# Optimization experiments

Hardware: AMD Instinct MI355X
Metric: run time of the kernel (lower is better)

## Reference

```python
import jax, jax.numpy as jnp
import numpy as np

N = 20000       # nodes per graph
E = 320000      # edges per graph (avg degree 16)
R = 8           # num_relations
B = 2           # batch of graphs
DIMS = [128, 256, 256, 128]  # in -> hidden -> hidden -> out
SLOPE = 0.2     # LeakyReLU negative slope


def setup_inputs() -> dict:
    key = jax.random.key(0)
    ks = jax.random.split(key, 12)
    inp = {
        "x": jax.random.normal(ks[0], (B, N, DIMS[0]), dtype=jnp.float32),
        "edge_index": jax.random.randint(ks[1], (B, 2, E), 0, N, dtype=jnp.int32),
        "edge_type": jax.random.randint(ks[2], (B, E), 0, R, dtype=jnp.int32),
    }
    for l in range(3):
        cin, cout = DIMS[l], DIMS[l + 1]
        s = 1.0 / np.sqrt(cin)
        inp[f"W{l}"] = jax.random.normal(ks[3 + 3 * l], (R, cin, cout), jnp.float32) * s
        inp[f"root{l}"] = jax.random.normal(ks[4 + 3 * l], (cin, cout), jnp.float32) * s
        inp[f"b{l}"] = jnp.zeros((cout,), jnp.float32)
    return inp


def _rgcn_layer(h, src, dst, etype, W, root, b):
    """One RGCNConv (per-relation mean aggregation) on a single graph.
    h: (N,Cin), src/dst/etype: (E,), W: (R,Cin,Cout), root: (Cin,Cout), b: (Cout,)
    """
    # transform every node by every relation weight once: (N,R,Cout)
    h_rel = jnp.einsum('nc,rcd->nrd', h, W)
    # per-edge message: gather source node transformed by that edge's relation
    msg = h_rel[src, etype]                               # (E,Cout)
    # per-(target-node, relation) mean, as in PyG's per-relation propagate
    seg = dst * R + etype                                 # (E,)
    sums = jax.ops.segment_sum(msg, seg, num_segments=N * R)
    cnt = jax.ops.segment_sum(jnp.ones((msg.shape[0],), h.dtype), seg,
                              num_segments=N * R)
    mean = sums / jnp.maximum(cnt, 1.0)[:, None]          # (N*R,Cout)
    agg = mean.reshape(N, R, -1).sum(axis=1)              # (N,Cout)
    return agg + h @ root + b


def reference(x, edge_index, edge_type, W0, root0, b0, W1, root1, b1, W2, root2, b2):
    params = [(W0, root0, b0), (W1, root1, b1), (W2, root2, b2)]

    def single(xg, ei, et):
        src, dst = ei[0], ei[1]
        h = xg
        for (W, root, b) in params:
            h = _rgcn_layer(h, src, dst, et, W, root, b)
            h = jnp.where(h > 0, h, SLOPE * h)  # LeakyReLU(0.2); dropout=identity (eval)
        return h

    return jax.vmap(single)(x, edge_index, edge_type)
```

## Files before the change

kernel.cpp:

```cpp
#include <hip/hip_runtime.h>
#include <hip/hip_bf16.h>

#define NN 20000
#define EE 320000
#define RR 8
#define NR (NN * RR)
#define NB 40
#define SCAP 640

typedef float f32x4 __attribute__((ext_vector_type(4)));
typedef short s16x8 __attribute__((ext_vector_type(8)));

__device__ __forceinline__ unsigned short f2bf(float f) {
  unsigned u = __builtin_bit_cast(unsigned, f);
  unsigned r = u + 0x7FFFu + ((u >> 16) & 1u);
  return (unsigned short)(r >> 16);
}
__device__ __forceinline__ float bf2f(unsigned short u) {
  return __builtin_bit_cast(float, (unsigned)u << 16);
}
__device__ __forceinline__ void gload_lds16(const void* g, void* l) {
  __builtin_amdgcn_global_load_lds(
      (const __attribute__((address_space(1))) unsigned*)g,
      (__attribute__((address_space(3))) unsigned*)l, 16, 0, 0);
}

__global__ void k_count(const int* __restrict__ ei, const int* __restrict__ et,
                        int* __restrict__ cnt) {
  int e = blockIdx.x * blockDim.x + threadIdx.x;
  int g = e >= EE;
  int el = e - g * EE;
  int d = ei[(size_t)g * 2 * EE + EE + el];
  int t = et[(size_t)g * EE + el];
  atomicAdd(&cnt[(size_t)g * NR + d * RR + t], 1);
}

__global__ __launch_bounds__(1024) void k_scan1(const int* __restrict__ cnt,
                                                int* __restrict__ off,
                                                int* __restrict__ btot) {
  int g = blockIdx.y, b = blockIdx.x;
  const int* c = cnt + (size_t)g * NR;
  int* o = off + (size_t)g * NR;
  __shared__ int wsum[16];
  int lane = threadIdx.x & 63, w = threadIdx.x >> 6;
  int i = b * 4096 + (int)threadIdx.x * 4;
  int4 v = {0, 0, 0, 0};
  if (i + 3 < NR) v = *(const int4*)&c[i];
  else {
    if (i < NR) v.x = c[i];
    if (i + 1 < NR) v.y = c[i + 1];
    if (i + 2 < NR) v.z = c[i + 2];
  }
  int s0 = v.x, s1 = s0 + v.y, s2 = s1 + v.z, s3 = s2 + v.w;
  int s = s3;
  for (int d = 1; d < 64; d <<= 1) {
    int t = __shfl_up(s, d);
    if (lane >= d) s += t;
  }
  if (lane == 63) wsum[w] = s;
  __syncthreads();
  if (threadIdx.x < 16) {
    int ws = wsum[threadIdx.x];
    for (int d = 1; d < 16; d <<= 1) {
      int t = __shfl_up(ws, d);
      if ((int)threadIdx.x >= d) ws += t;
    }
    wsum[threadIdx.x] = ws;
  }
  __syncthreads();
  int excl = (w > 0 ? wsum[w - 1] : 0) + (s - s3);
  if (i < NR) o[i] = excl;
  if (i + 1 < NR) o[i + 1] = excl + s0;
  if (i + 2 < NR) o[i + 2] = excl + s1;
  if (i + 3 < NR) o[i + 3] = excl + s2;
  if (threadIdx.x == 0) btot[g * NB + b] = wsum[15];
}

__global__ void k_scan2(const int* __restrict__ btot, int* __restrict__ bof) {
  int g = threadIdx.x >> 6, lane = threadIdx.x & 63;
  int v = (lane < NB) ? btot[g * NB + lane] : 0;
  int s = v;
  for (int d = 1; d < 64; d <<= 1) {
    int t = __shfl_up(s, d);
    if (lane >= d) s += t;
  }
  if (lane < NB) bof[g * NB + lane] = s - v;
}

__global__ __launch_bounds__(1024) void k_scan3(int* __restrict__ off,
                                                const int* __restrict__ bof) {
  int g = blockIdx.y;
  int add = bof[g * NB + blockIdx.x];
  int i = blockIdx.x * 4096 + (int)threadIdx.x * 4;
  int* o = off + (size_t)g * NR;
  if (i + 3 < NR) {
    int4 v = *(const int4*)&o[i];
    v.x += add; v.y += add; v.z += add; v.w += add;
    *(int4*)&o[i] = v;
  } else {
    for (int j = i; j < NR; ++j) o[j] += add;
  }
}

__global__ void k_scatter(const int* __restrict__ ei, const int* __restrict__ et,
                          int* __restrict__ off, int* __restrict__ ssrc) {
  int e = blockIdx.x * blockDim.x + threadIdx.x;
  int g = e >= EE;
  int el = e - g * EE;
  int s = ei[(size_t)g * 2 * EE + el];
  int d = ei[(size_t)g * 2 * EE + EE + el];
  int t = et[(size_t)g * EE + el];
  int pos = atomicAdd(&off[(size_t)g * NR + d * RR + t], 1);
  ssrc[(size_t)g * EE + pos] = s;
}

__global__ void k_cvt(const float* __restrict__ x, unsigned short* __restrict__ hX) {
  int i = (blockIdx.x * blockDim.x + threadIdx.x) * 4;
  if (i >= 2 * NN * 128) return;
  int g = i >= NN * 128;
  int il = i - g * NN * 128;
  float4 v = *(const float4*)&x[i];
  ushort4 o;
  o.x = f2bf(v.x); o.y = f2bf(v.y); o.z = f2bf(v.z); o.w = f2bf(v.w);
  *(ushort4*)&hX[(size_t)g * NN * 256 + il] = o;
}

__global__ void k_btf(const float* __restrict__ W, const float* __restrict__ root,
                      unsigned short* __restrict__ btf, int Cin, int Cout,
                      int Ktot) {
  int idx = blockIdx.x * blockDim.x + threadIdx.x;
  if (idx >= Cout * Ktot) return;
  int j = idx & 7;
  int lane = (idx >> 3) & 63;
  int kk = (idx >> 9) & 1;
  int t = idx >> 10;
  int fr = t % (Cout / 16);
  int s = t / (Cout / 16);
  int co = fr * 16 + (lane & 15);
  int k = s * 64 + kk * 32 + (lane >> 4) * 8 + j;
  int r = k / Cin, ci = k - r * Cin;
  float v = (r < RR) ? W[((size_t)r * Cin + ci) * Cout + co]
                     : root[(size_t)ci * Cout + co];
  btf[idx] = f2bf(v);
}

#define LOADB(bb, s)                                                           \
  _Pragma("unroll") for (int kk = 0; kk < 2; ++kk)                             \
      _Pragma("unroll") for (int f = 0; f < 4; ++f) bb[kk][f] =                \
          *(const s16x8*)(btl +                                                \
                          (size_t)(((s) * (COUT / 16) + wn16 + f) * 2 + kk) *  \
                              512);

#define COPYB()                                                                \
  _Pragma("unroll") for (int kk = 0; kk < 2; ++kk)                             \
      _Pragma("unroll") for (int f = 0; f < 4; ++f) bc[kk][f] = bn[kk][f];

#define MFMA_STEP_C(Ab, c, bb)                                                 \
  do {                                                                         \
    _Pragma("unroll") for (int kk = 0; kk < 2; ++kk) {                         \
      s16x8 a[MF];                                                             \
      _Pragma("unroll") for (int f = 0; f < MF; ++f) {                         \
        int row = wm + f * 16 + (lane & 15);                                   \
        int colb = kk * 64 + (lane >> 4) * 16;                                 \
        a[f] = *(const s16x8*)((Ab) + (c)*ASTR + row * 128 +                   \
                               (colb ^ ((row & 7) << 4)));                     \
      }                                                                        \
      _Pragma("unroll") for (int fm = 0; fm < MF; ++fm)                        \
          _Pragma("unroll") for (int fn = 0; fn < 4; ++fn)                     \
              acc[fm][fn] = __builtin_amdgcn_mfma_f32_16x16x32_bf16(           \
                  a[fm], bb[kk][fn], acc[fm][fn], 0, 0, 0);                    \
    }                                                                          \
  } while (0)

#define ACC4(u)                                                                \
  {                                                                            \
    faH[c][0] += __builtin_bit_cast(float, (u).x & 0xFFFF0000u);               \
    faL[c][0] += __builtin_bit_cast(float, (u).x << 16);                       \
    faH[c][1] += __builtin_bit_cast(float, (u).y & 0xFFFF0000u);               \
    faL[c][1] += __builtin_bit_cast(float, (u).y << 16);                       \
    faH[c][2] += __builtin_bit_cast(float, (u).z & 0xFFFF0000u);               \
    faL[c][2] += __builtin_bit_cast(float, (u).z << 16);                       \
    faH[c][3] += __builtin_bit_cast(float, (u).w & 0xFFFF0000u);               \
    faL[c][3] += __builtin_bit_cast(float, (u).w << 16);                       \
  }

template <int CIN, int COUT, bool OUTF32>
__global__ __launch_bounds__(256) void k_fused(
    const int* __restrict__ ssrc, const int* __restrict__ off,
    const unsigned short* __restrict__ h, const unsigned short* __restrict__ btf,
    const float* __restrict__ bias, void* __restrict__ outp) {
  constexpr int KTOT = (RR + 1) * CIN;
  constexpr int NS = KTOT / 64;
  constexpr int CH = CIN / 64;
  constexpr int CPT = CIN / 8;
  constexpr int NCH = CPT / 8;
  constexpr int NWN = COUT / 64;
  constexpr int MW = 4 / NWN;
  constexpr int WR = 32 / MW;
  constexpr int MF = WR / 16;
  constexpr int ASTR = 4112;
  __shared__ char As[2][CH * ASTR];
  __shared__ int offs[32][9];
  __shared__ int sseg[SCAP];
  const int tid = threadIdx.x, lane = tid & 63, wave = tid >> 6;
  const int wn = (wave % NWN) * 64;
  const int wn16 = wn >> 4;
  const int wm = (wave / NWN) * WR;
  const int m0 = blockIdx.x * 32;
  const int g = blockIdx.z;
  ssrc += (size_t)g * EE;
  off += (size_t)g * NR;
  h += (size_t)g * NN * 256;

  for (int idx = tid; idx < 32 * 9; idx += 256) {
    int row = idx / 9, j = idx - row * 9;
    int seg0 = (m0 + row) * RR;
    offs[row][j] = (j == 0) ? (seg0 == 0 ? 0 : off[seg0 - 1]) : off[seg0 + j - 1];
  }
  const int segA = m0 * RR;
  const int ebase = (segA == 0) ? 0 : off[segA - 1];
  const int eend = off[(m0 + 32) * RR - 1];
  const int cntE = eend - ebase;
  const bool inl = cntE <= SCAP;
  if (inl)
    for (int i = tid; i < cntE; i += 256) sseg[i] = ssrc[ebase + i];
  __syncthreads();

  f32x4 acc[MF][4] = {};
  const int arow = tid >> 3;
  const int q = tid & 7;
  const int swzA = (arow & 7) << 4;
  const unsigned short* hq = h + q * CPT;
  const unsigned short* btl = btf + lane * 8;

  auto produce = [&](int r, int buf) {
    float faL[NCH][4], faH[NCH][4];
#pragma unroll
    for (int c = 0; c < NCH; ++c)
#pragma unroll
      for (int w = 0; w < 4; ++w) { faL[c][w] = 0.f; faH[c][w] = 0.f; }
    int o0 = offs[arow][r], o1 = offs[arow][r + 1];
    int e = o0;
    for (; e + 1 < o1; e += 2) {
      int sa = inl ? sseg[e - ebase] : ssrc[e];
      int sb = inl ? sseg[e + 1 - ebase] : ssrc[e + 1];
      const unsigned short* pa = hq + (size_t)sa * CIN;
      const unsigned short* pb = hq + (size_t)sb * CIN;
#pragma unroll
      for (int c = 0; c < NCH; ++c) {
        uint4 ua = *(const uint4*)(pa + c * 8);
        uint4 ub = *(const uint4*)(pb + c * 8);
        ACC4(ua);
        ACC4(ub);
      }
    }
    if (e < o1) {
      int sa = inl ? sseg[e - ebase] : ssrc[e];
      const unsigned short* pa = hq + (size_t)sa * CIN;
#pragma unroll
      for (int c = 0; c < NCH; ++c) {
        uint4 ua = *(const uint4*)(pa + c * 8);
        ACC4(ua);
      }
    }
    float inv = 1.0f / fmaxf((float)(o1 - o0), 1.0f);
#pragma unroll
    for (int c = 0; c < NCH; ++c) {
      s16x8 mbv;
#pragma unroll
      for (int w = 0; w < 4; ++w) {
        mbv[2 * w] = (short)f2bf(faL[c][w] * inv);
        mbv[2 * w + 1] = (short)f2bf(faH[c][w] * inv);
      }
      int colb = (q * CPT + c * 8) * 2;
      int ct = colb >> 7;
      int wb = colb & 127;
      *(s16x8*)(As[buf] + ct * ASTR + arow * 128 + (wb ^ swzA)) = mbv;
    }
  };

  auto root_stage = [&]() {
#pragma unroll
    for (int i = 0; i < CH; ++i) {
      int o = i * ASTR + wave * 1024;
      int ob = wave * 1024 + lane * 16;
      int row = (ob >> 7) & 31;
      int wb = ob & 127;
      gload_lds16((const char*)h + ((size_t)(m0 + row) * CIN + i * 64) * 2 +
                      (wb ^ ((row & 7) << 4)),
                  As[RR & 1] + o);
    }
  };

  s16x8 bc[2][4], bn[2][4];
  LOADB(bc, 0);
  produce(0, 0);
  __syncthreads();

  for (int r = 0; r <= RR; ++r) {
    const char* Ab = As[r & 1];
#pragma unroll
    for (int c = 0; c < CH; ++c) {
      int s = r * CH + c;
      if (s + 1 < NS) { LOADB(bn, s + 1); }
      MFMA_STEP_C(Ab, c, bc);
      if (s + 1 < NS) { COPYB(); }
    }
    if (r + 1 < RR) produce(r + 1, (r + 1) & 1);
    else if (r + 1 == RR) root_stage();
    __syncthreads();
  }

#pragma unroll
  for (int fm = 0; fm < MF; ++fm) {
    int rbase = m0 + wm + fm * 16 + (lane >> 4) * 4;
#pragma unroll
    for (int fn = 0; fn < 4; ++fn) {
      int col = wn + fn * 16 + (lane & 15);
      float bv = bias[col];
#pragma unroll
      for (int v = 0; v < 4; ++v) {
        int row = rbase + v;
        float xv = acc[fm][fn][v] + bv;
        xv = xv > 0.f ? xv : 0.2f * xv;
        if constexpr (OUTF32)
          ((float*)outp)[(size_t)g * NN * COUT + (size_t)row * COUT + col] = xv;
        else
          ((unsigned short*)outp)[(size_t)g * NN * 256 + (size_t)row * COUT +
                                  col] = f2bf(xv);
      }
    }
  }
}

extern "C" void kernel_launch(void* const* d_in, const int* in_sizes, int n_in,
                              void* d_out, int out_size, void* d_ws, size_t ws_size,
                              hipStream_t stream) {
  const float* x  = (const float*)d_in[0];
  const int* ei   = (const int*)d_in[1];
  const int* etp  = (const int*)d_in[2];
  const float* W0 = (const float*)d_in[3];
  const float* r0 = (const float*)d_in[4];
  const float* b0 = (const float*)d_in[5];
  const float* W1 = (const float*)d_in[6];
  const float* r1 = (const float*)d_in[7];
  const float* b1 = (const float*)d_in[8];
  const float* W2 = (const float*)d_in[9];
  const float* r2 = (const float*)d_in[10];
  const float* b2 = (const float*)d_in[11];

  char* p = (char*)d_ws;
  unsigned short* hX  = (unsigned short*)p; p += (size_t)2 * NN * 256 * 2;
  unsigned short* h_a = (unsigned short*)p; p += (size_t)2 * NN * 256 * 2;
  int* cnt  = (int*)p; p += (size_t)2 * NR * 4;
  int* off  = (int*)p; p += (size_t)2 * NR * 4;
  int* btot = (int*)p; p += (size_t)2 * NB * 4;
  int* bof  = (int*)p; p += (size_t)2 * NB * 4;
  int* ssrc = (int*)p; p += (size_t)2 * EE * 4;
  unsigned short* bt0 = (unsigned short*)p; p += (size_t)256 * 1152 * 2;
  unsigned short* bt1 = (unsigned short*)p; p += (size_t)256 * 2304 * 2;
  unsigned short* bt2 = (unsigned short*)p; p += (size_t)128 * 2304 * 2;

  k_btf<<<(256 * 1152 + 255) / 256, 256, 0, stream>>>(W0, r0, bt0, 128, 256, 1152);
  k_btf<<<(256 * 2304 + 255) / 256, 256, 0, stream>>>(W1, r1, bt1, 256, 256, 2304);
  k_btf<<<(128 * 2304 + 255) / 256, 256, 0, stream>>>(W2, r2, bt2, 256, 128, 2304);

  (void)hipMemsetAsync(cnt, 0, (size_t)2 * NR * 4, stream);
  k_count<<<2 * EE / 256, 256, 0, stream>>>(ei, etp, cnt);
  k_scan1<<<dim3(NB, 2), 1024, 0, stream>>>(cnt, off, btot);
  k_scan2<<<1, 128, 0, stream>>>(btot, bof);
  k_scan3<<<dim3(NB, 2), 1024, 0, stream>>>(off, bof);
  k_cvt<<<2 * NN * 128 / 4 / 256, 256, 0, stream>>>(x, hX);
  k_scatter<<<2 * EE / 256, 256, 0, stream>>>(ei, etp, off, ssrc);

  k_fused<128, 256, false><<<dim3(625, 1, 2), 256, 0, stream>>>(
      ssrc, off, hX, bt0, b0, h_a);
  k_fused<256, 256, false><<<dim3(625, 1, 2), 256, 0, stream>>>(
      ssrc, off, h_a, bt1, b1, hX);
  k_fused<256, 128, true><<<dim3(625, 1, 2), 256, 0, stream>>>(
      ssrc, off, hX, bt2, b2, d_out);
}
```

Baseline: 387.4 us.

## Process both graphs per block with 512 threads to share weight-fragment loads

Each fused block now covers the same 32-row node tile of both graphs (64 rows, 8 waves), so every B-fragment load of the packed weights serves twice as many MFMA rows. Source indices are pre-shifted into byte offsets in shared memory, and the B double-buffer is ping-ponged across two k-steps instead of being copied each step. In exchange, shared memory and register use per block roughly double and there are half as many blocks, which can lower occupancy and latency hiding for the gather phase.

After: 473.4 us. 22.2% more time.

```diff
diff --git a/kernel.cpp b/kernel.cpp
--- a/kernel.cpp
+++ b/kernel.cpp
@@ -151,10 +151,6 @@
                           (size_t)(((s) * (COUT / 16) + wn16 + f) * 2 + kk) *  \
                               512);
 
-#define COPYB()                                                                \
-  _Pragma("unroll") for (int kk = 0; kk < 2; ++kk)                             \
-      _Pragma("unroll") for (int f = 0; f < 4; ++f) bc[kk][f] = bn[kk][f];
-
 #define MFMA_STEP_C(Ab, c, bb)                                                 \
   do {                                                                         \
     _Pragma("unroll") for (int kk = 0; kk < 2; ++kk) {                         \
@@ -185,7 +181,7 @@
   }
 
 template <int CIN, int COUT, bool OUTF32>
-__global__ __launch_bounds__(256) void k_fused(
+__global__ __launch_bounds__(512) void k_fused(
     const int* __restrict__ ssrc, const int* __restrict__ off,
     const unsigned short* __restrict__ h, const unsigned short* __restrict__ btf,
     const float* __restrict__ bias, void* __restrict__ outp) {
@@ -195,42 +191,48 @@
   constexpr int CPT = CIN / 8;
   constexpr int NCH = CPT / 8;
   constexpr int NWN = COUT / 64;
-  constexpr int MW = 4 / NWN;
-  constexpr int WR = 32 / MW;
+  constexpr int MW = 8 / NWN;
+  constexpr int WR = 64 / MW;
   constexpr int MF = WR / 16;
-  constexpr int ASTR = 4112;
+  constexpr int ASTR = 64 * 128 + 16;
+  constexpr int SH = (CIN == 256) ? 9 : 8;
   __shared__ char As[2][CH * ASTR];
-  __shared__ int offs[32][9];
-  __shared__ int sseg[SCAP];
+  __shared__ int offs[64][9];
+  __shared__ int sseg[2 * SCAP];
   const int tid = threadIdx.x, lane = tid & 63, wave = tid >> 6;
   const int wn = (wave % NWN) * 64;
   const int wn16 = wn >> 4;
   const int wm = (wave / NWN) * WR;
   const int m0 = blockIdx.x * 32;
-  const int g = blockIdx.z;
-  ssrc += (size_t)g * EE;
-  off += (size_t)g * NR;
-  h += (size_t)g * NN * 256;
-
-  for (int idx = tid; idx < 32 * 9; idx += 256) {
+
+  for (int idx = tid; idx < 64 * 9; idx += 512) {
     int row = idx / 9, j = idx - row * 9;
-    int seg0 = (m0 + row) * RR;
-    offs[row][j] = (j == 0) ? (seg0 == 0 ? 0 : off[seg0 - 1]) : off[seg0 + j - 1];
-  }
-  const int segA = m0 * RR;
-  const int ebase = (segA == 0) ? 0 : off[segA - 1];
-  const int eend = off[(m0 + 32) * RR - 1];
-  const int cntE = eend - ebase;
-  const bool inl = cntE <= SCAP;
-  if (inl)
-    for (int i = tid; i < cntE; i += 256) sseg[i] = ssrc[ebase + i];
+    const int* offg = off + (size_t)(row >> 5) * NR;
+    int seg0 = (m0 + (row & 31)) * RR;
+    offs[row][j] = (j == 0) ? (seg0 == 0 ? 0 : offg[seg0 - 1]) : offg[seg0 + j - 1];
+  }
+  const int eb0 = (m0 == 0) ? 0 : off[m0 * RR - 1];
+  const int ee0 = off[(m0 + 32) * RR - 1];
+  const int eb1 = (m0 == 0) ? 0 : off[NR + m0 * RR - 1];
+  const int ee1 = off[NR + (m0 + 32) * RR - 1];
+  const bool inl0 = (ee0 - eb0) <= SCAP, inl1 = (ee1 - eb1) <= SCAP;
+  if (inl0)
+    for (int i = tid; i < ee0 - eb0; i += 512) sseg[i] = ssrc[eb0 + i] << SH;
+  if (inl1)
+    for (int i = tid; i < ee1 - eb1; i += 512)
+      sseg[SCAP + i] = ssrc[(size_t)EE + eb1 + i] << SH;
   __syncthreads();
 
   f32x4 acc[MF][4] = {};
   const int arow = tid >> 3;
   const int q = tid & 7;
   const int swzA = (arow & 7) << 4;
-  const unsigned short* hq = h + q * CPT;
+  const int gw = arow >> 5;
+  const int ebg = gw ? eb1 : eb0;
+  const bool inlg = gw ? inl1 : inl0;
+  const int* ssrcg = ssrc + (size_t)gw * EE;
+  const int* ssegg = sseg + gw * SCAP;
+  const char* hqB = (const char*)(h + (size_t)gw * NN * 256) + (size_t)q * CPT * 2;
   const unsigned short* btl = btf + lane * 8;
 
   auto produce = [&](int r, int buf) {
@@ -242,10 +244,10 @@
     int o0 = offs[arow][r], o1 = offs[arow][r + 1];
     int e = o0;
     for (; e + 1 < o1; e += 2) {
-      int sa = inl ? sseg[e - ebase] : ssrc[e];
-      int sb = inl ? sseg[e + 1 - ebase] : ssrc[e + 1];
-      const unsigned short* pa = hq + (size_t)sa * CIN;
-      const unsigned short* pb = hq + (size_t)sb * CIN;
+      int soA = inlg ? ssegg[e - ebg] : (ssrcg[e] << SH);
+      int soB = inlg ? ssegg[e + 1 - ebg] : (ssrcg[e + 1] << SH);
+      const unsigned short* pa = (const unsigned short*)(hqB + soA);
+      const unsigned short* pb = (const unsigned short*)(hqB + soB);
 #pragma unroll
       for (int c = 0; c < NCH; ++c) {
         uint4 ua = *(const uint4*)(pa + c * 8);
@@ -255,8 +257,8 @@
       }
     }
     if (e < o1) {
-      int sa = inl ? sseg[e - ebase] : ssrc[e];
-      const unsigned short* pa = hq + (size_t)sa * CIN;
+      int soA = inlg ? ssegg[e - ebg] : (ssrcg[e] << SH);
+      const unsigned short* pa = (const unsigned short*)(hqB + soA);
 #pragma unroll
       for (int c = 0; c < NCH; ++c) {
         uint4 ua = *(const uint4*)(pa + c * 8);
@@ -284,9 +286,12 @@
     for (int i = 0; i < CH; ++i) {
       int o = i * ASTR + wave * 1024;
       int ob = wave * 1024 + lane * 16;
-      int row = (ob >> 7) & 31;
+      int row = (ob >> 7) & 63;
       int wb = ob & 127;
-      gload_lds16((const char*)h + ((size_t)(m0 + row) * CIN + i * 64) * 2 +
+      int g = row >> 5;
+      int gr = m0 + (row & 31);
+      gload_lds16((const char*)h +
+                      ((size_t)g * NN * 256 + (size_t)gr * CIN + i * 64) * 2 +
                       (wb ^ ((row & 7) << 4)),
                   As[RR & 1] + o);
     }
@@ -300,11 +305,12 @@
   for (int r = 0; r <= RR; ++r) {
     const char* Ab = As[r & 1];
 #pragma unroll
-    for (int c = 0; c < CH; ++c) {
+    for (int c = 0; c < CH; c += 2) {
       int s = r * CH + c;
       if (s + 1 < NS) { LOADB(bn, s + 1); }
       MFMA_STEP_C(Ab, c, bc);
-      if (s + 1 < NS) { COPYB(); }
+      if (s + 2 < NS) { LOADB(bc, s + 2); }
+      MFMA_STEP_C(Ab, c + 1, bn);
     }
     if (r + 1 < RR) produce(r + 1, (r + 1) & 1);
     else if (r + 1 == RR) root_stage();
@@ -313,20 +319,21 @@
 
 #pragma unroll
   for (int fm = 0; fm < MF; ++fm) {
-    int rbase = m0 + wm + fm * 16 + (lane >> 4) * 4;
 #pragma unroll
     for (int fn = 0; fn < 4; ++fn) {
       int col = wn + fn * 16 + (lane & 15);
       float bv = bias[col];
 #pragma unroll
       for (int v = 0; v < 4; ++v) {
-        int row = rbase + v;
+        int asrow = wm + fm * 16 + (lane >> 4) * 4 + v;
+        int og = asrow >> 5;
+        int row = m0 + (asrow & 31);
         float xv = acc[fm][fn][v] + bv;
         xv = xv > 0.f ? xv : 0.2f * xv;
         if constexpr (OUTF32)
-          ((float*)outp)[(size_t)g * NN * COUT + (size_t)row * COUT + col] = xv;
+          ((float*)outp)[(size_t)og * NN * COUT + (size_t)row * COUT + col] = xv;
         else
-          ((unsigned short*)outp)[(size_t)g * NN * 256 + (size_t)row * COUT +
+          ((unsigned short*)outp)[(size_t)og * NN * 256 + (size_t)row * COUT +
                                   col] = f2bf(xv);
       }
     }
@@ -373,10 +380,7 @@
   k_cvt<<<2 * NN * 128 / 4 / 256, 256, 0, stream>>>(x, hX);
   k_scatter<<<2 * EE / 256, 256, 0, stream>>>(ei, etp, off, ssrc);
 
-  k_fused<128, 256, false><<<dim3(625, 1, 2), 256, 0, stream>>>(
-      ssrc, off, hX, bt0, b0, h_a);
-  k_fused<256, 256, false><<<dim3(625, 1, 2), 256, 0, stream>>>(
-      ssrc, off, h_a, bt1, b1, hX);
-  k_fused<256, 128, true><<<dim3(625, 1, 2), 256, 0, stream>>>(
-      ssrc, off, hX, bt2, b2, d_out);
-}
+  k_fused<128, 256, false><<<625, 512, 0, stream>>>(ssrc, off, hX, bt0, b0, h_a);
+  k_fused<256, 256, false><<<625, 512, 0, stream>>>(ssrc, off, h_a, bt1, b1, hX);
+  k_fused<256, 128, true><<<625, 512, 0, stream>>>(ssrc, off, hX, bt2, b2, d_out);
+}
```
